# Kernel optimization log

Hardware: AMD Instinct MI355X
Metric: run time of the kernel (lower is better)

Reference implementation:

```python
import jax, jax.numpy as jnp
import numpy as np

NUM_FIELDS = 16
EMBED = 32
W1 = 7
W2 = 5
VOCAB = 100000
BATCH = 4096
K1 = NUM_FIELDS // 2  # first k-max pool size (num_inputs/2)
K2 = 3                # second k-max pool size
DN = ('NHWC', 'HWIO', 'NHWC')


def kmax_pool_last(x, k):
    # k-max pooling along the last axis (tf.nn.top_k values)
    return jax.lax.top_k(x, k)[0]


def setup_inputs() -> dict:
    key = jax.random.key(0)
    ks = jax.random.split(key, 6)
    return {
        'idx': jax.random.randint(ks[0], (BATCH, NUM_FIELDS), 0, VOCAB),
        'w0': jax.random.normal(ks[1], (NUM_FIELDS, VOCAB, EMBED), jnp.float32) * 0.02,
        'b0': jnp.zeros((NUM_FIELDS, EMBED), jnp.float32),
        'f1': jax.random.normal(ks[2], (EMBED, W1, 1, 2), jnp.float32) * 0.1,
        'f2': jax.random.normal(ks[3], (EMBED, W2, 2, 2), jnp.float32) * 0.1,
        'w1': jax.random.normal(ks[4], (2 * 3 * EMBED, 1), jnp.float32) * 0.02,
        'b1': jnp.zeros((1,), jnp.float32),
    }


def reference(idx, w0, b0, f1, f2, w1, b1):
    # sparse one-hot matmul == embedding row gather: [B, F, E]
    emb = w0[jnp.arange(NUM_FIELDS)[None, :], idx] + b0[None, :, :]
    l = jnp.tanh(emb)  # layer_acts[0] = tanh; dropout identity at test
    # reshape [-1, F, E, 1] then transpose [0,2,1,3] -> [B, E, F, 1]
    l = jnp.transpose(l[..., None], (0, 2, 1, 3))
    # conv1: kernel [E, W1, 1, 2], SAME -> [B, E, F, 2]
    l = jax.lax.conv_general_dilated(l, f1, (1, 1), 'SAME', dimension_numbers=DN)
    # k-max pool over field axis (last axis after transpose) -> [B, E, K1, 2]
    l = jnp.transpose(kmax_pool_last(jnp.transpose(l, (0, 1, 3, 2)), K1), (0, 1, 3, 2))
    # conv2: kernel [E, W2, 2, 2], SAME -> [B, E, K1, 2]
    l = jax.lax.conv_general_dilated(l, f2, (1, 1), 'SAME', dimension_numbers=DN)
    # second k-max pool -> [B, E, 3, 2]
    l = jnp.transpose(kmax_pool_last(jnp.transpose(l, (0, 1, 3, 2)), K2), (0, 1, 3, 2))
    l = jnp.tanh(l.reshape(l.shape[0], EMBED * 3 * 2))  # layer_acts[1] = tanh
    logits = (l @ w1 + b1).reshape(-1)  # layer_acts[2] = none
    return jax.nn.sigmoid(logits)  # y_prob
```

## Files before the change

kernel.cpp:

```cpp
#include <hip/hip_runtime.h>
#include <math.h>

#define NF 16
#define VOCAB 100000
#define TSH 40
#define NROW 63

typedef _Float16 half8 __attribute__((ext_vector_type(8)));
typedef _Float16 half4 __attribute__((ext_vector_type(4)));

__device__ __forceinline__ float tanhf_fast(float x) {
    float e = __expf(2.f * x);
    return 1.f - 2.f * __builtin_amdgcn_rcpf(e + 1.f);
}

__global__ __launch_bounds__(64, 6) void ccpm_fwd(
    const int* __restrict__ idx,
    const float* __restrict__ w0,
    const float* __restrict__ b0,
    const float* __restrict__ f1,
    const float* __restrict__ f2,
    const float* __restrict__ w1,
    const float* __restrict__ b1,
    float* __restrict__ out)
{
    const int b = blockIdx.x;
    const int l = threadIdx.x;

    __shared__ __align__(16) _Float16 buf[NROW * TSH + 8];

    const float4 z4 = make_float4(0.f, 0.f, 0.f, 0.f);
    float4* bz = (float4*)buf;

    #pragma unroll
    for (int i = 0; i < 5; ++i) {
        int n = i * 64 + l;
        if (n < (NROW * TSH + 8) / 8) bz[n] = z4;
    }
    __syncthreads();

    {
        int f  = l >> 2;
        int e0 = (l & 3) * 8;
        int row = idx[b * NF + f];
        const float4* src = (const float4*)(w0 + ((size_t)f * VOCAB + row) * 32 + e0);
        const float4* bb  = (const float4*)(b0 + f * 32 + e0);
        float4 v0 = src[0], v1 = src[1];
        float4 u0 = bb[0],  u1 = bb[1];
        float g[8];
        g[0]=v0.x+u0.x; g[1]=v0.y+u0.y; g[2]=v0.z+u0.z; g[3]=v0.w+u0.w;
        g[4]=v1.x+u1.x; g[5]=v1.y+u1.y; g[6]=v1.z+u1.z; g[7]=v1.w+u1.w;
        #pragma unroll
        for (int i = 0; i < 8; ++i)
            buf[(e0 + i + 15) * TSH + f + 3] = (_Float16)tanhf_fast(g[i]);
    }
    __syncthreads();

    const int h  = l >> 1;
    const int wh = l & 1;

    float a0[8], a1[8];
    {
        #pragma unroll
        for (int w = 0; w < 8; ++w) { a0[w] = 0.f; a1[w] = 0.f; }
        const float2* f1v = (const float2*)f1;
        #pragma unroll 2
        for (int kh = 0; kh < 32; ++kh) {
            const half8* r = (const half8*)&buf[(h + kh) * TSH + 8 * wh];
            half8 wa = r[0];
            half8 wbv = r[1];
            float win[16];
            #pragma unroll
            for (int i = 0; i < 8; ++i) { win[i] = (float)wa[i]; win[8 + i] = (float)wbv[i]; }
            #pragma unroll
            for (int kw = 0; kw < 7; ++kw) {
                float2 fp = f1v[kh * 7 + kw];
                #pragma unroll
                for (int w = 0; w < 8; ++w) {
                    a0[w] += win[w + kw] * fp.x;
                    a1[w] += win[w + kw] * fp.y;
                }
            }
        }
    }
    __syncthreads();

    #pragma unroll
    for (int i = 0; i < 5; ++i) {
        int n = i * 64 + l;
        if (n < (NROW * TSH + 8) / 8) bz[n] = z4;
    }
    __syncthreads();

    {
        float own[8], recv[8];
        #pragma unroll
        for (int i = 0; i < 8; ++i) {
            own[i]  = wh ? a1[i] : a0[i];
            recv[i] = __shfl_xor(wh ? a0[i] : a1[i], 1, 64);
        }
        float v[16];
        #pragma unroll
        for (int i = 0; i < 8; ++i) {
            v[i]     = wh ? recv[i] : own[i];
            v[8 + i] = wh ? own[i] : recv[i];
        }
        int r[16];
        #pragma unroll
        for (int i = 0; i < 16; ++i) r[i] = 0;
        #pragma unroll
        for (int i = 0; i < 16; ++i)
            #pragma unroll
            for (int j = i + 1; j < 16; ++j) {
                bool ge = v[i] >= v[j];
                r[j] += ge ? 1 : 0;
                r[i] += ge ? 0 : 1;
            }
        #pragma unroll
        for (int i = 0; i < 16; ++i)
            if (r[i] < 8) buf[(h + 15) * TSH + wh * 12 + 2 + r[i]] = (_Float16)v[i];
    }
    __syncthreads();

    float c0[4], c1[4];
    {
        #pragma unroll
        for (int w = 0; w < 4; ++w) { c0[w] = 0.f; c1[w] = 0.f; }
        const float4* f2q = (const float4*)f2;
        #pragma unroll 2
        for (int kh = 0; kh < 32; ++kh) {
            const _Float16* rw = &buf[(h + kh) * TSH];
            half4 p0a = *(const half4*)(rw + 4 * wh);
            half4 p0b = *(const half4*)(rw + 4 * wh + 4);
            half4 p1a = *(const half4*)(rw + 12 + 4 * wh);
            half4 p1b = *(const half4*)(rw + 16 + 4 * wh);
            float q0[8], q1[8];
            #pragma unroll
            for (int i = 0; i < 4; ++i) {
                q0[i] = (float)p0a[i]; q0[4 + i] = (float)p0b[i];
                q1[i] = (float)p1a[i]; q1[4 + i] = (float)p1b[i];
            }
            #pragma unroll
            for (int kw = 0; kw < 5; ++kw) {
                float4 fp = f2q[kh * 5 + kw];
                #pragma unroll
                for (int w = 0; w < 4; ++w) {
                    c0[w] += q0[w + kw] * fp.x + q1[w + kw] * fp.z;
                    c1[w] += q0[w + kw] * fp.y + q1[w + kw] * fp.w;
                }
            }
        }
    }

    {
        float own[4], recv[4];
        #pragma unroll
        for (int i = 0; i < 4; ++i) {
            own[i]  = wh ? c1[i] : c0[i];
            recv[i] = __shfl_xor(wh ? c0[i] : c1[i], 1, 64);
        }
        float v[8];
        #pragma unroll
        for (int i = 0; i < 4; ++i) {
            v[i]     = wh ? recv[i] : own[i];
            v[4 + i] = wh ? own[i] : recv[i];
        }
        int r[8];
        #pragma unroll
        for (int i = 0; i < 8; ++i) r[i] = 0;
        #pragma unroll
        for (int i = 0; i < 8; ++i)
            #pragma unroll
            for (int j = i + 1; j < 8; ++j) {
                bool ge = v[i] >= v[j];
                r[j] += ge ? 1 : 0;
                r[i] += ge ? 0 : 1;
            }
        float t0 = 0.f, t1 = 0.f, t2 = 0.f;
        #pragma unroll
        for (int i = 0; i < 8; ++i) {
            t0 = (r[i] == 0) ? v[i] : t0;
            t1 = (r[i] == 1) ? v[i] : t1;
            t2 = (r[i] == 2) ? v[i] : t2;
        }
        float s = tanhf_fast(t0) * w1[h * 6 + wh]
                + tanhf_fast(t1) * w1[h * 6 + 2 + wh]
                + tanhf_fast(t2) * w1[h * 6 + 4 + wh];
        #pragma unroll
        for (int off = 32; off; off >>= 1) s += __shfl_xor(s, off, 64);
        if (l == 0) {
            float logit = s + b1[0];
            out[b] = __builtin_amdgcn_rcpf(1.f + __expf(-logit));
        }
    }
}

extern "C" void kernel_launch(void* const* d_in, const int* in_sizes, int n_in,
                              void* d_out, int out_size, void* d_ws, size_t ws_size,
                              hipStream_t stream) {
    const int*   idx = (const int*)d_in[0];
    const float* w0  = (const float*)d_in[1];
    const float* b0  = (const float*)d_in[2];
    const float* f1  = (const float*)d_in[3];
    const float* f2  = (const float*)d_in[4];
    const float* w1  = (const float*)d_in[5];
    const float* b1  = (const float*)d_in[6];
    float* out = (float*)d_out;
    ccpm_fwd<<<out_size, 64, 0, stream>>>(idx, w0, b0, f1, f2, w1, b1, out);
}
```

Measured before the change: 294.4 us.

## Use packed fp16 dot2 for convolutions with pair-interleaved LDS layout

Repacks the LDS activations into fp16 pairs along the kernel-height axis, with a duplicated odd-shifted plane for conv1, so each conv inner step becomes a v_dot2 fp16 instruction instead of two scalar FMAs after fp16-to-fp32 conversions. A small pre-kernel packs the f1/f2 filters into half2 pairs in workspace. This roughly halves the conv arithmetic and removes conversion work. The costs are a larger LDS footprint (occupancy hint lowered from 6 to 4), an extra kernel launch, and fp16 rounding of the filter weights.

```diff
diff --git a/kernel.cpp b/kernel.cpp
--- a/kernel.cpp
+++ b/kernel.cpp
@@ -3,39 +3,71 @@
 
 #define NF 16
 #define VOCAB 100000
-#define TSH 40
-#define NROW 63
-
-typedef _Float16 half8 __attribute__((ext_vector_type(8)));
-typedef _Float16 half4 __attribute__((ext_vector_type(4)));
+#define S1 28
+#define NP1 31
+#define PB 868
+#define S2 20
+#define LDSW 1736
+
+typedef _Float16 h2 __attribute__((ext_vector_type(2)));
+
+#if __has_builtin(__builtin_amdgcn_fdot2)
+#define FDOT2(a, b, c) __builtin_amdgcn_fdot2((a), (b), (c), false)
+#else
+#define FDOT2(a, b, c) ((float)(a)[0] * (float)(b)[0] + ((float)(a)[1] * (float)(b)[1] + (c)))
+#endif
 
 __device__ __forceinline__ float tanhf_fast(float x) {
     float e = __expf(2.f * x);
     return 1.f - 2.f * __builtin_amdgcn_rcpf(e + 1.f);
 }
 
-__global__ __launch_bounds__(64, 6) void ccpm_fwd(
+__device__ __forceinline__ h2 u2h(unsigned int u) {
+    union { unsigned int u; h2 h; } c; c.u = u; return c.h;
+}
+
+__global__ void pack_filters(const float* __restrict__ f1,
+                             const float* __restrict__ f2,
+                             unsigned int* __restrict__ ws) {
+    int t = threadIdx.x;
+    if (t < 224) {
+        int j = t / 14, r = t % 14, kw = r >> 1, o = r & 1;
+        h2 h;
+        h[0] = (_Float16)f1[((2 * j) * 7 + kw) * 2 + o];
+        h[1] = (_Float16)f1[((2 * j + 1) * 7 + kw) * 2 + o];
+        union { h2 h; unsigned int u; } c; c.h = h;
+        ws[t] = c.u;
+    }
+    for (int n = t; n < 320; n += 256) {
+        int kh = n / 10, r = n % 10, kw = r >> 1, o = r & 1;
+        h2 h;
+        h[0] = (_Float16)f2[(kh * 5 + kw) * 4 + o];
+        h[1] = (_Float16)f2[(kh * 5 + kw) * 4 + 2 + o];
+        union { h2 h; unsigned int u; } c; c.h = h;
+        ws[256 + n] = c.u;
+    }
+}
+
+__global__ __launch_bounds__(64, 4) void ccpm_fwd(
     const int* __restrict__ idx,
     const float* __restrict__ w0,
     const float* __restrict__ b0,
-    const float* __restrict__ f1,
-    const float* __restrict__ f2,
     const float* __restrict__ w1,
     const float* __restrict__ b1,
+    const unsigned int* __restrict__ FP,
     float* __restrict__ out)
 {
     const int b = blockIdx.x;
     const int l = threadIdx.x;
 
-    __shared__ __align__(16) _Float16 buf[NROW * TSH + 8];
+    __shared__ __align__(16) unsigned int lds[LDSW];
 
     const float4 z4 = make_float4(0.f, 0.f, 0.f, 0.f);
-    float4* bz = (float4*)buf;
 
     #pragma unroll
-    for (int i = 0; i < 5; ++i) {
+    for (int i = 0; i < 7; ++i) {
         int n = i * 64 + l;
-        if (n < (NROW * TSH + 8) / 8) bz[n] = z4;
+        if (n < LDSW / 4) ((float4*)lds)[n] = z4;
     }
     __syncthreads();
 
@@ -50,9 +82,16 @@
         float g[8];
         g[0]=v0.x+u0.x; g[1]=v0.y+u0.y; g[2]=v0.z+u0.z; g[3]=v0.w+u0.w;
         g[4]=v1.x+u1.x; g[5]=v1.y+u1.y; g[6]=v1.z+u1.z; g[7]=v1.w+u1.w;
-        #pragma unroll
-        for (int i = 0; i < 8; ++i)
-            buf[(e0 + i + 15) * TSH + f + 3] = (_Float16)tanhf_fast(g[i]);
+        _Float16* H = (_Float16*)lds;
+        const int C = f + 3;
+        #pragma unroll
+        for (int i = 0; i < 8; ++i) {
+            int R = e0 + i + 15;
+            _Float16 hv = (_Float16)tanhf_fast(g[i]);
+            H[((R >> 1) * S1 + C) * 2 + (R & 1)] = hv;
+            int prB = (R & 1) ? (R >> 1) : (R >> 1) - 1;
+            H[(PB + prB * S1 + C) * 2 + ((R & 1) ^ 1)] = hv;
+        }
     }
     __syncthreads();
 
@@ -63,22 +102,25 @@
     {
         #pragma unroll
         for (int w = 0; w < 8; ++w) { a0[w] = 0.f; a1[w] = 0.f; }
-        const float2* f1v = (const float2*)f1;
+        const unsigned int* plane = lds + ((h & 1) ? PB : 0);
+        const int pr0 = h >> 1;
+        const int wb  = wh * 8;
         #pragma unroll 2
-        for (int kh = 0; kh < 32; ++kh) {
-            const half8* r = (const half8*)&buf[(h + kh) * TSH + 8 * wh];
-            half8 wa = r[0];
-            half8 wbv = r[1];
-            float win[16];
-            #pragma unroll
-            for (int i = 0; i < 8; ++i) { win[i] = (float)wa[i]; win[8 + i] = (float)wbv[i]; }
+        for (int j = 0; j < 16; ++j) {
+            const uint4* rp = (const uint4*)(plane + (pr0 + j) * S1 + wb);
+            uint4 q0 = rp[0], q1 = rp[1], q2 = rp[2], q3 = rp[3];
+            unsigned int win[16] = {q0.x,q0.y,q0.z,q0.w, q1.x,q1.y,q1.z,q1.w,
+                                    q2.x,q2.y,q2.z,q2.w, q3.x,q3.y,q3.z,q3.w};
+            const unsigned int* ft = FP + j * 14;
             #pragma unroll
             for (int kw = 0; kw < 7; ++kw) {
-                float2 fp = f1v[kh * 7 + kw];
+                h2 f0 = u2h(ft[kw * 2 + 0]);
+                h2 f1h = u2h(ft[kw * 2 + 1]);
                 #pragma unroll
                 for (int w = 0; w < 8; ++w) {
-                    a0[w] += win[w + kw] * fp.x;
-                    a1[w] += win[w + kw] * fp.y;
+                    h2 wv = u2h(win[w + kw]);
+                    a0[w] = FDOT2(wv, f0, a0[w]);
+                    a1[w] = FDOT2(wv, f1h, a1[w]);
                 }
             }
         }
@@ -88,7 +130,7 @@
     #pragma unroll
     for (int i = 0; i < 5; ++i) {
         int n = i * 64 + l;
-        if (n < (NROW * TSH + 8) / 8) bz[n] = z4;
+        if (n < (63 * S2) / 4) ((float4*)lds)[n] = z4;
     }
     __syncthreads();
 
@@ -116,9 +158,11 @@
                 r[j] += ge ? 1 : 0;
                 r[i] += ge ? 0 : 1;
             }
+        _Float16* H = (_Float16*)lds;
         #pragma unroll
         for (int i = 0; i < 16; ++i)
-            if (r[i] < 8) buf[(h + 15) * TSH + wh * 12 + 2 + r[i]] = (_Float16)v[i];
+            if (r[i] < 8)
+                H[((h + 15) * S2 + (r[i] + 2)) * 2 + wh] = (_Float16)v[i];
     }
     __syncthreads();
 
@@ -126,27 +170,22 @@
     {
         #pragma unroll
         for (int w = 0; w < 4; ++w) { c0[w] = 0.f; c1[w] = 0.f; }
-        const float4* f2q = (const float4*)f2;
+        const int wb2 = wh * 4;
         #pragma unroll 2
         for (int kh = 0; kh < 32; ++kh) {
-            const _Float16* rw = &buf[(h + kh) * TSH];
-            half4 p0a = *(const half4*)(rw + 4 * wh);
-            half4 p0b = *(const half4*)(rw + 4 * wh + 4);
-            half4 p1a = *(const half4*)(rw + 12 + 4 * wh);
-            half4 p1b = *(const half4*)(rw + 16 + 4 * wh);
-            float q0[8], q1[8];
-            #pragma unroll
-            for (int i = 0; i < 4; ++i) {
-                q0[i] = (float)p0a[i]; q0[4 + i] = (float)p0b[i];
-                q1[i] = (float)p1a[i]; q1[4 + i] = (float)p1b[i];
-            }
+            const uint4* rp = (const uint4*)(lds + (h + kh) * S2 + wb2);
+            uint4 qa = rp[0], qb = rp[1];
+            unsigned int q[8] = {qa.x,qa.y,qa.z,qa.w, qb.x,qb.y,qb.z,qb.w};
+            const unsigned int* ft = FP + 256 + kh * 10;
             #pragma unroll
             for (int kw = 0; kw < 5; ++kw) {
-                float4 fp = f2q[kh * 5 + kw];
+                h2 f0 = u2h(ft[kw * 2 + 0]);
+                h2 f1h = u2h(ft[kw * 2 + 1]);
                 #pragma unroll
                 for (int w = 0; w < 4; ++w) {
-                    c0[w] += q0[w + kw] * fp.x + q1[w + kw] * fp.z;
-                    c1[w] += q0[w + kw] * fp.y + q1[w + kw] * fp.w;
+                    h2 wv = u2h(q[w + kw]);
+                    c0[w] = FDOT2(wv, f0, c0[w]);
+                    c1[w] = FDOT2(wv, f1h, c1[w]);
                 }
             }
         }
@@ -206,5 +245,8 @@
     const float* w1  = (const float*)d_in[5];
     const float* b1  = (const float*)d_in[6];
     float* out = (float*)d_out;
-    ccpm_fwd<<<out_size, 64, 0, stream>>>(idx, w0, b0, f1, f2, w1, b1, out);
-}
+    unsigned int* ws = (unsigned int*)d_ws;
+
+    pack_filters<<<1, 256, 0, stream>>>(f1, f2, ws);
+    ccpm_fwd<<<out_size, 64, 0, stream>>>(idx, w0, b0, w1, b1, ws, out);
+}
```

New measurement: 279.1 us. -5.2%, faster.
